# Kernel tuning notes

Hardware: AMD Instinct MI355X
Metric: run time of the kernel (lower is better)

Reference implementation:

```python
import jax, jax.numpy as jnp
import numpy as np

B, N, C = 2, 2048, 768
H = 12
HD = C // H
SCALE = HD ** -0.5


def setup_inputs() -> dict:
    key = jax.random.key(0)
    ks = jax.random.split(key, 5)
    s = 1.0 / np.sqrt(C)
    return {
        "x": jax.random.normal(ks[0], (B, N, C), dtype=jnp.float32),
        "Wq": jax.random.normal(ks[1], (C, C), dtype=jnp.float32) * s,
        "Wk": jax.random.normal(ks[2], (C, C), dtype=jnp.float32) * s,
        "Wv": jax.random.normal(ks[3], (C, C), dtype=jnp.float32) * s,
        "Wo": jax.random.normal(ks[4], (C, C), dtype=jnp.float32) * s,
        "bo": jnp.zeros((C,), dtype=jnp.float32),
    }


def reference(x, Wq, Wk, Wv, Wo, bo):
    b, n, c = x.shape
    # projections (equinox Linear: y = W @ x, i.e. x @ W.T); split heads -> [b, h, n, hd]
    q = (x @ Wq.T).reshape(b, n, H, HD).transpose(0, 2, 1, 3)
    k = (x @ Wk.T).reshape(b, n, H, HD).transpose(0, 2, 1, 3)
    v = (x @ Wv.T).reshape(b, n, H, HD).transpose(0, 2, 1, 3)
    # full O(N^2) score matrix, scaled dot-product
    scores = jnp.einsum("bhqd,bhkd->bhqk", q, k) * SCALE  # [b, h, n, n]
    probs = jax.nn.softmax(scores, axis=-1)
    # attn_drop = 0.0 -> identity
    out = jnp.einsum("bhqk,bhkd->bhqd", probs, v)  # [b, h, n, hd]
    out = out.transpose(0, 2, 1, 3).reshape(b, n, c)
    # output projection (proj_drop = 0.0 -> identity)
    return out @ Wo.T + bo
```

## Files before the change

kernel.cpp:

```cpp
#include <hip/hip_runtime.h>
#include <hip/hip_bf16.h>
#include <cstdint>

typedef __bf16 bf16;
typedef bf16 bf16x8 __attribute__((ext_vector_type(8)));
typedef float f32x4 __attribute__((ext_vector_type(4)));
typedef uint32_t u32;

#define MFMA16(a, b, c) __builtin_amdgcn_mfma_f32_16x16x32_bf16(a, b, c, 0, 0, 0)

static constexpr int Bb = 2, Hh = 12, Nn = 2048, Cc = 768, HD = 64;
static constexpr float SCALE_L2E = 0.125f * 1.4426950408889634f;

__device__ inline u32 pkbf(float a, float b) {
    union { struct { uint16_t lo, hi; } s; u32 w; } u;
    u.s.lo = __builtin_bit_cast(uint16_t, (bf16)a);
    u.s.hi = __builtin_bit_cast(uint16_t, (bf16)b);
    return u.w;
}

__device__ __forceinline__ size_t fidx(int bh, int n, int hd) {
    return ((size_t)(bh * 128 + (n >> 4)) * 2 + (hd >> 5)) * 512 +
           (size_t)(((hd >> 3) & 3) * 128 + (n & 15) * 8 + (hd & 7));
}
__device__ __forceinline__ size_t vidx(int bh, int n, int hd) {
    return (((size_t)(bh * 32 + (n >> 6)) * 4 + (hd >> 4)) * 2 + ((n >> 5) & 1)) * 512 +
           (size_t)(((n >> 3) & 3) * 128 + (hd & 15) * 8 + (n & 7));
}

__device__ __forceinline__ void stage16(const bf16* g, bf16* l) {
    __builtin_amdgcn_global_load_lds(
        (const __attribute__((address_space(1))) void*)g,
        (__attribute__((address_space(3))) void*)l, 16, 0, 0);
}

__device__ __forceinline__ void gload(bf16x8& d, const bf16* p) {
    asm volatile("global_load_dwordx4 %0, %1, off" : "=v"(d) : "v"(p));
}

#define VMWAIT(N) do { asm volatile("s_waitcnt vmcnt(" #N ")" ::); \
                       __builtin_amdgcn_sched_barrier(0); } while (0)

__global__ __launch_bounds__(256) void cvt_all(const float* __restrict__ x,
                                               const float* __restrict__ wq,
                                               const float* __restrict__ wk,
                                               const float* __restrict__ wv,
                                               const float* __restrict__ wo,
                                               bf16* __restrict__ xb,
                                               bf16* __restrict__ wqkv,
                                               bf16* __restrict__ wob) {
    const int b = blockIdx.x;
    const float* src;
    bf16* dst;
    int i;
    if (b < 1536) {
        src = x; dst = xb; i = b * 256 + threadIdx.x;
    } else {
        const int wbid  = b - 1536;
        const int which = wbid / 288;
        src = which == 0 ? wq : which == 1 ? wk : which == 2 ? wv : wo;
        dst = which == 3 ? wob : wqkv + (size_t)which * 589824;
        i = (wbid % 288) * 256 + threadIdx.x;
    }
    const float4* p = reinterpret_cast<const float4*>(src) + (size_t)i * 2;
    float4 v0 = p[0], v1 = p[1];
    bf16x8 o;
    o[0] = (bf16)v0.x; o[1] = (bf16)v0.y; o[2] = (bf16)v0.z; o[3] = (bf16)v0.w;
    o[4] = (bf16)v1.x; o[5] = (bf16)v1.y; o[6] = (bf16)v1.z; o[7] = (bf16)v1.w;
    reinterpret_cast<bf16x8*>(dst)[i] = o;
}

__global__ __launch_bounds__(256, 3) void gemm_qkv(const bf16* __restrict__ X,
                                                   const bf16* __restrict__ W,
                                                   bf16* __restrict__ QF,
                                                   bf16* __restrict__ KF,
                                                   bf16* __restrict__ VF) {
    const int m0      = blockIdx.x * 128;
    const int j00     = blockIdx.y * 128;
    const int grp     = blockIdx.y / 6;
    const int colbase = (blockIdx.y % 6) * 128;
    const int w   = threadIdx.x >> 6;
    const int wr  = w >> 1;
    const int wc  = w & 1;
    const int l   = threadIdx.x & 63;
    const int lr  = l & 15;
    const int lg  = l >> 4;

    __shared__ bf16 lsA[2][128 * 32];
    __shared__ bf16 lsB[2][128 * 32];

    const int lrow = l >> 2;
    const int lcol = (l & 3) * 8;

    auto STAGE = [&](int buf, int kk) {
#pragma unroll
        for (int i = 0; i < 2; i++) {
            const int s = w * 2 + i;
            stage16(X + (size_t)(m0 + s * 16 + lrow) * Cc + kk + lcol, &lsA[buf][s * 512]);
            stage16(W + (size_t)(j00 + s * 16 + lrow) * Cc + kk + lcol, &lsB[buf][s * 512]);
        }
    };

    f32x4 acc[4][4] = {};

    STAGE(0, 0);
    __syncthreads();
    int cur = 0;
#pragma unroll 1
    for (int it = 0; it < 24; ++it) {
        if (it < 23) STAGE(cur ^ 1, (it + 1) * 32);
        bf16x8 a[4], b[4];
#pragma unroll
        for (int r = 0; r < 4; r++)
            a[r] = *reinterpret_cast<const bf16x8*>(&lsA[cur][(wr * 64 + r * 16 + lr) * 32 + lg * 8]);
#pragma unroll
        for (int c = 0; c < 4; c++)
            b[c] = *reinterpret_cast<const bf16x8*>(&lsB[cur][(wc * 64 + c * 16 + lr) * 32 + lg * 8]);
        __builtin_amdgcn_s_setprio(1);
#pragma unroll
        for (int r = 0; r < 4; r++)
#pragma unroll
            for (int c = 0; c < 4; c++)
                acc[r][c] = MFMA16(a[r], b[c], acc[r][c]);
        __builtin_amdgcn_s_setprio(0);
        __syncthreads();
        cur ^= 1;
    }

#pragma unroll
    for (int r = 0; r < 4; r++)
#pragma unroll
        for (int c = 0; c < 4; c++)
#pragma unroll
            for (int j = 0; j < 4; j++) {
                const int m   = m0 + wr * 64 + r * 16 + lg * 4 + j;
                const int col = colbase + wc * 64 + c * 16 + lr;
                const int bb = m >> 11, n = m & 2047;
                const int h = col >> 6, hd = col & 63;
                const int bh = bb * Hh + h;
                const float v = acc[r][c][j];
                if (grp == 0) {
                    QF[fidx(bh, n, hd)] = (bf16)(v * SCALE_L2E);
                } else if (grp == 1) {
                    KF[fidx(bh, n, hd)] = (bf16)v;
                } else {
                    VF[vidx(bh, n, hd)] = (bf16)v;
                }
            }
}

__global__ __launch_bounds__(256) void gemm_proj(const bf16* __restrict__ X,
                                                 const bf16* __restrict__ W,
                                                 const float* __restrict__ bias,
                                                 float* __restrict__ Y) {
    const int m0 = blockIdx.x * 64;
    const int j0 = blockIdx.y * 64;
    const int w  = threadIdx.x >> 6;
    const int l  = threadIdx.x & 63;
    const int lr = l & 15;
    const int lg = l >> 4;

    __shared__ bf16 lsA[2][64 * 32];
    __shared__ bf16 lsB[2][64 * 32];

    const int lrow = l >> 2;
    const int lcol = (l & 3) * 8;

    auto STAGE = [&](int buf, int kk) {
        stage16(X + (size_t)(m0 + w * 16 + lrow) * Cc + kk + lcol, &lsA[buf][w * 512]);
        stage16(W + (size_t)(j0 + w * 16 + lrow) * Cc + kk + lcol, &lsB[buf][w * 512]);
    };

    f32x4 acc[4] = {};

    STAGE(0, 0);
    __syncthreads();
    int cur = 0;
#pragma unroll 1
    for (int it = 0; it < 24; ++it) {
        if (it < 23) STAGE(cur ^ 1, (it + 1) * 32);
        bf16x8 a = *reinterpret_cast<const bf16x8*>(&lsA[cur][(w * 16 + lr) * 32 + lg * 8]);
        bf16x8 b[4];
#pragma unroll
        for (int c = 0; c < 4; c++)
            b[c] = *reinterpret_cast<const bf16x8*>(&lsB[cur][(c * 16 + lr) * 32 + lg * 8]);
        __builtin_amdgcn_s_setprio(1);
#pragma unroll
        for (int c = 0; c < 4; c++)
            acc[c] = MFMA16(a, b[c], acc[c]);
        __builtin_amdgcn_s_setprio(0);
        __syncthreads();
        cur ^= 1;
    }

    const int mw = m0 + w * 16;
#pragma unroll
    for (int c = 0; c < 4; c++)
#pragma unroll
        for (int j = 0; j < 4; j++) {
            const int m   = mw + lg * 4 + j;
            const int col = j0 + c * 16 + lr;
            Y[(size_t)m * Cc + col] = acc[c][j] + bias[col];
        }
}

__global__ __launch_bounds__(256, 3) void attn_kernel(const bf16* __restrict__ QF,
                                                      const bf16* __restrict__ KF,
                                                      const bf16* __restrict__ VF,
                                                      bf16* __restrict__ AO) {
    const int bid = (blockIdx.x & 7) * 96 + (blockIdx.x >> 3);
    const int qb  = bid & 31;
    const int bh  = bid >> 5;
    const int tid = threadIdx.x;
    const int wid = tid >> 6;
    const int l   = tid & 63;
    const int lr  = l & 15;
    const int lg  = l >> 4;

    __shared__ bf16 vbuf[3][4096];
    __shared__ u32  p_lds[4][576];

    f32x4 acc[4] = {};
    f32x4 accs = {0.f, 0.f, 0.f, 0.f};

    const bf16* Qp = QF + ((size_t)(bh * 128 + qb * 4 + wid) * 2) * 512 + l * 8;
    const bf16x8 qf0 = *reinterpret_cast<const bf16x8*>(Qp);
    const bf16x8 qf1 = *reinterpret_cast<const bf16x8*>(Qp + 512);

    bf16x8 ONES;
#pragma unroll
    for (int i = 0; i < 8; i++) ONES[i] = (bf16)1.0f;

    bf16x8 ka[8];

    auto loadK = [&](int t) {
        const bf16* p = KF + ((size_t)bh * 256 + t * 8) * 512 + l * 8;
#pragma unroll
        for (int s = 0; s < 8; s++)
            gload(ka[s], p + (size_t)s * 512);
    };
    auto stageV = [&](int slot, int t) {
        const size_t tb = ((size_t)bh * 256 + t * 8) * 512;
#pragma unroll
        for (int i = 0; i < 2; i++) {
            const int s = wid * 2 + i;
            stage16(VF + tb + (size_t)s * 512 + l * 8, &vbuf[slot][s * 512]);
        }
    };

    const f32x4 fz = {0.f, 0.f, 0.f, 0.f};

    auto BODY = [&](int t, bool prefetchK) {
        f32x4 s[4];
        __builtin_amdgcn_s_setprio(1);
#pragma unroll
        for (int st = 0; st < 4; st++) {
            s[st] = MFMA16(ka[st * 2], qf0, fz);
            s[st] = MFMA16(ka[st * 2 + 1], qf1, s[st]);
        }
        __builtin_amdgcn_s_setprio(0);
        if (prefetchK) loadK(t + 1);

#pragma unroll
        for (int st = 0; st < 4; st++) {
            float p0 = exp2f(s[st][0]);
            float p1 = exp2f(s[st][1]);
            float p2 = exp2f(s[st][2]);
            float p3 = exp2f(s[st][3]);
            *reinterpret_cast<uint2*>(&p_lds[wid][lr * 36 + st * 8 + lg * 2]) =
                make_uint2(pkbf(p0, p1), pkbf(p2, p3));
        }
        asm volatile("s_waitcnt lgkmcnt(0)" ::: "memory");
        __builtin_amdgcn_sched_barrier(0);
        const bf16x8 pa0 = *reinterpret_cast<const bf16x8*>(&p_lds[wid][lr * 36 + lg * 4]);
        const bf16x8 pa1 = *reinterpret_cast<const bf16x8*>(&p_lds[wid][lr * 36 + 16 + lg * 4]);

        const bf16* vb = &vbuf[t % 3][l * 8];
        __builtin_amdgcn_s_setprio(1);
#pragma unroll
        for (int c = 0; c < 4; c++) {
            bf16x8 v0 = *reinterpret_cast<const bf16x8*>(vb + (c * 2) * 512);
            bf16x8 v1 = *reinterpret_cast<const bf16x8*>(vb + (c * 2 + 1) * 512);
            acc[c] = MFMA16(v0, pa0, acc[c]);
            acc[c] = MFMA16(v1, pa1, acc[c]);
        }
        accs = MFMA16(ONES, pa0, accs);
        accs = MFMA16(ONES, pa1, accs);
        __builtin_amdgcn_s_setprio(0);
    };

    stageV(0, 0);
    loadK(0);
    stageV(1, 1);

#pragma unroll 1
    for (int t = 0; t < 31; ++t) {
        VMWAIT(2);
        __builtin_amdgcn_s_barrier();
        BODY(t, true);
        if (t <= 29) stageV((t + 2) % 3, t + 2);
    }
    VMWAIT(0);
    __builtin_amdgcn_s_barrier();
    BODY(31, false);
    __builtin_amdgcn_s_barrier();

    float* o_lds = reinterpret_cast<float*>(&vbuf[0][0]) + wid * 1088;
    const float rinv = 1.0f / accs[0];
#pragma unroll
    for (int c = 0; c < 4; c++)
#pragma unroll
        for (int j = 0; j < 4; j++)
            o_lds[(c * 16 + lg * 4 + j) * 17 + lr] = acc[c][j] * rinv;
    asm volatile("s_waitcnt lgkmcnt(0)" ::: "memory");
    __builtin_amdgcn_sched_barrier(0);

    const int bb = bh / Hh, h = bh % Hh;
    const int q0 = qb * 64 + wid * 16;
    const int qq = l >> 2, dc = (l & 3) * 16;
    bf16x8 o0, o1;
#pragma unroll
    for (int dd = 0; dd < 8; dd++) o0[dd] = (bf16)o_lds[(dc + dd) * 17 + qq];
#pragma unroll
    for (int dd = 0; dd < 8; dd++) o1[dd] = (bf16)o_lds[(dc + 8 + dd) * 17 + qq];
    bf16* dst = AO + ((size_t)(bb * Nn) + q0 + qq) * Cc + h * 64 + dc;
    *reinterpret_cast<bf16x8*>(dst) = o0;
    *reinterpret_cast<bf16x8*>(dst + 8) = o1;
}

extern "C" void kernel_launch(void* const* d_in, const int* in_sizes, int n_in,
                              void* d_out, int out_size, void* d_ws, size_t ws_size,
                              hipStream_t stream) {
    const float* x  = (const float*)d_in[0];
    const float* Wq = (const float*)d_in[1];
    const float* Wk = (const float*)d_in[2];
    const float* Wv = (const float*)d_in[3];
    const float* Wo = (const float*)d_in[4];
    const float* bo = (const float*)d_in[5];

    const size_t XB    = 0;
    const size_t WQKVB = XB + 6291456;
    const size_t WOB   = WQKVB + 3538944;
    const size_t QB    = WOB + 1179648;
    const size_t KB    = QB + 6291456;
    const size_t VTB   = KB + 6291456;
    const size_t AOB   = VTB + 6291456;
    const size_t NEED  = AOB + 6291456;
    if (ws_size < NEED) return;

    char* ws = (char*)d_ws;
    bf16* xb   = (bf16*)(ws + XB);
    bf16* wqkv = (bf16*)(ws + WQKVB);
    bf16* wob  = (bf16*)(ws + WOB);
    bf16* QF   = (bf16*)(ws + QB);
    bf16* KF   = (bf16*)(ws + KB);
    bf16* VF   = (bf16*)(ws + VTB);
    bf16* AOb  = (bf16*)(ws + AOB);

    cvt_all<<<2688, 256, 0, stream>>>(x, Wq, Wk, Wv, Wo, xb, wqkv, wob);

    gemm_qkv<<<dim3(32, 18), 256, 0, stream>>>(xb, wqkv, QF, KF, VF);

    attn_kernel<<<768, 256, 0, stream>>>(QF, KF, VF, AOb);

    gemm_proj<<<dim3(64, 12), 256, 0, stream>>>(AOb, wob, bo, (float*)d_out);
}
```

Measured before the change: 99.74 us.

## Split attention KV loop across two wave teams and merge partial sums

Doubles the attention block to 512 threads. Two teams of four waves each process half of the key/value sequence for the same 64 queries, and team 1's partial accumulators and row sums are merged through LDS at the end. The V staging pipeline changes from a triple buffer with wait-count 2 to a per-team double buffer with full VMWAIT(0) each step. This shortens each block's serial loop and adds parallelism, at the cost of a merge step, more LDS per block, and less prefetch depth. Softmax needs no rescaling because scores are used without a max subtraction.

```diff
diff --git a/kernel.cpp b/kernel.cpp
--- a/kernel.cpp
+++ b/kernel.cpp
@@ -204,26 +204,28 @@
         }
 }
 
-__global__ __launch_bounds__(256, 3) void attn_kernel(const bf16* __restrict__ QF,
+__global__ __launch_bounds__(512, 4) void attn_kernel(const bf16* __restrict__ QF,
                                                       const bf16* __restrict__ KF,
                                                       const bf16* __restrict__ VF,
                                                       bf16* __restrict__ AO) {
-    const int bid = (blockIdx.x & 7) * 96 + (blockIdx.x >> 3);
-    const int qb  = bid & 31;
-    const int bh  = bid >> 5;
-    const int tid = threadIdx.x;
-    const int wid = tid >> 6;
-    const int l   = tid & 63;
-    const int lr  = l & 15;
-    const int lg  = l >> 4;
-
-    __shared__ bf16 vbuf[3][4096];
-    __shared__ u32  p_lds[4][576];
+    const int bid  = (blockIdx.x & 7) * 96 + (blockIdx.x >> 3);
+    const int qb   = bid & 31;
+    const int bh   = bid >> 5;
+    const int tid  = threadIdx.x;
+    const int wid  = tid >> 6;
+    const int team = wid >> 2;
+    const int wt   = wid & 3;
+    const int l    = tid & 63;
+    const int lr   = l & 15;
+    const int lg   = l >> 4;
+
+    __shared__ bf16 vbuf[2][2][4096];
+    __shared__ u32  p_lds[8][576];
 
     f32x4 acc[4] = {};
     f32x4 accs = {0.f, 0.f, 0.f, 0.f};
 
-    const bf16* Qp = QF + ((size_t)(bh * 128 + qb * 4 + wid) * 2) * 512 + l * 8;
+    const bf16* Qp = QF + ((size_t)(bh * 128 + qb * 4 + wt) * 2) * 512 + l * 8;
     const bf16x8 qf0 = *reinterpret_cast<const bf16x8*>(Qp);
     const bf16x8 qf1 = *reinterpret_cast<const bf16x8*>(Qp + 512);
 
@@ -233,24 +235,33 @@
 
     bf16x8 ka[8];
 
+    const int tbase = team * 16;
+
     auto loadK = [&](int t) {
-        const bf16* p = KF + ((size_t)bh * 256 + t * 8) * 512 + l * 8;
+        const bf16* p = KF + ((size_t)bh * 256 + (tbase + t) * 8) * 512 + l * 8;
 #pragma unroll
         for (int s = 0; s < 8; s++)
             gload(ka[s], p + (size_t)s * 512);
     };
     auto stageV = [&](int slot, int t) {
-        const size_t tb = ((size_t)bh * 256 + t * 8) * 512;
+        const size_t tb = ((size_t)bh * 256 + (tbase + t) * 8) * 512;
 #pragma unroll
         for (int i = 0; i < 2; i++) {
-            const int s = wid * 2 + i;
-            stage16(VF + tb + (size_t)s * 512 + l * 8, &vbuf[slot][s * 512]);
+            const int s = wt * 2 + i;
+            stage16(VF + tb + (size_t)s * 512 + l * 8, &vbuf[team][slot][s * 512]);
         }
     };
 
     const f32x4 fz = {0.f, 0.f, 0.f, 0.f};
 
-    auto BODY = [&](int t, bool prefetchK) {
+    stageV(0, 0);
+    loadK(0);
+
+#pragma unroll 1
+    for (int t = 0; t < 16; ++t) {
+        VMWAIT(0);
+        __builtin_amdgcn_s_barrier();
+
         f32x4 s[4];
         __builtin_amdgcn_s_setprio(1);
 #pragma unroll
@@ -259,7 +270,10 @@
             s[st] = MFMA16(ka[st * 2 + 1], qf1, s[st]);
         }
         __builtin_amdgcn_s_setprio(0);
-        if (prefetchK) loadK(t + 1);
+        if (t < 15) {
+            loadK(t + 1);
+            stageV((t + 1) & 1, t + 1);
+        }
 
 #pragma unroll
         for (int st = 0; st < 4; st++) {
@@ -275,7 +289,7 @@
         const bf16x8 pa0 = *reinterpret_cast<const bf16x8*>(&p_lds[wid][lr * 36 + lg * 4]);
         const bf16x8 pa1 = *reinterpret_cast<const bf16x8*>(&p_lds[wid][lr * 36 + 16 + lg * 4]);
 
-        const bf16* vb = &vbuf[t % 3][l * 8];
+        const bf16* vb = &vbuf[team][t & 1][l * 8];
         __builtin_amdgcn_s_setprio(1);
 #pragma unroll
         for (int c = 0; c < 4; c++) {
@@ -287,26 +301,30 @@
         accs = MFMA16(ONES, pa0, accs);
         accs = MFMA16(ONES, pa1, accs);
         __builtin_amdgcn_s_setprio(0);
-    };
-
-    stageV(0, 0);
-    loadK(0);
-    stageV(1, 1);
-
-#pragma unroll 1
-    for (int t = 0; t < 31; ++t) {
-        VMWAIT(2);
-        __builtin_amdgcn_s_barrier();
-        BODY(t, true);
-        if (t <= 29) stageV((t + 2) % 3, t + 2);
-    }
-    VMWAIT(0);
-    __builtin_amdgcn_s_barrier();
-    BODY(31, false);
-    __builtin_amdgcn_s_barrier();
-
-    float* o_lds = reinterpret_cast<float*>(&vbuf[0][0]) + wid * 1088;
-    const float rinv = 1.0f / accs[0];
+    }
+
+    __syncthreads();
+    float* mrg = reinterpret_cast<float*>(&p_lds[0][0]);
+    if (team == 1) {
+        float* slot = mrg + wt * 1088 + l * 17;
+#pragma unroll
+        for (int c = 0; c < 4; c++)
+#pragma unroll
+            for (int j = 0; j < 4; j++) slot[c * 4 + j] = acc[c][j];
+        slot[16] = accs[0];
+    }
+    __syncthreads();
+    if (team == 1) return;
+
+    const float* slot = mrg + wt * 1088 + l * 17;
+#pragma unroll
+    for (int c = 0; c < 4; c++)
+#pragma unroll
+        for (int j = 0; j < 4; j++) acc[c][j] += slot[c * 4 + j];
+    const float rtot = accs[0] + slot[16];
+
+    float* o_lds = reinterpret_cast<float*>(&vbuf[0][0][0]) + wt * 1088;
+    const float rinv = 1.0f / rtot;
 #pragma unroll
     for (int c = 0; c < 4; c++)
 #pragma unroll
@@ -316,7 +334,7 @@
     __builtin_amdgcn_sched_barrier(0);
 
     const int bb = bh / Hh, h = bh % Hh;
-    const int q0 = qb * 64 + wid * 16;
+    const int q0 = qb * 64 + wt * 16;
     const int qq = l >> 2, dc = (l & 3) * 16;
     bf16x8 o0, o1;
 #pragma unroll
@@ -361,7 +379,7 @@
 
     gemm_qkv<<<dim3(32, 18), 256, 0, stream>>>(xb, wqkv, QF, KF, VF);
 
-    attn_kernel<<<768, 256, 0, stream>>>(QF, KF, VF, AOb);
+    attn_kernel<<<768, 512, 0, stream>>>(QF, KF, VF, AOb);
 
     gemm_proj<<<dim3(64, 12), 256, 0, stream>>>(AOb, wob, bo, (float*)d_out);
 }
```

Result: slower. 101.8 us (+2.1%).
